# Optimization experiments

Measured on AMD Instinct MI355X. Metric: run time of the kernel, lower is better.

Reference implementation:

```python
import jax, jax.numpy as jnp
import numpy as np

N, E, HID, H, L = 50000, 100000, 128, 4, 3
C = HID          # out_channels per head (concat=True -> H*C = 512)
ED = 1           # edge_dim
HC = H * C


def setup_inputs() -> dict:
    key = jax.random.key(0)
    ks = jax.random.split(key, 20)
    s = 0.05
    w = lambda k, shape: (jax.random.normal(k, shape, jnp.float32) * s)
    inp = {
        'x': jax.random.normal(ks[0], (N, HID), jnp.float32),
        'edge_index': jax.random.randint(ks[1], (2, E), 0, N),
        'edge_attr': jax.random.normal(ks[2], (E, ED), jnp.float32),
        # per-layer stacked parameters (TransformerConv + proj + LayerNorm)
        'Wq': w(ks[3], (L, HID, HC)), 'bq': jnp.zeros((L, HC), jnp.float32),
        'Wk': w(ks[4], (L, HID, HC)), 'bk': jnp.zeros((L, HC), jnp.float32),
        'Wv': w(ks[5], (L, HID, HC)), 'bv': jnp.zeros((L, HC), jnp.float32),
        'We': w(ks[6], (L, ED, HC)),                       # lin_edge, bias=False
        'Wskip': w(ks[7], (L, HID, HC)), 'bskip': jnp.zeros((L, HC), jnp.float32),
        'Wproj': w(ks[8], (L, HC, HID)), 'bproj': jnp.zeros((L, HID), jnp.float32),
        'gamma': jnp.ones((L, HID), jnp.float32), 'beta': jnp.zeros((L, HID), jnp.float32),
    }
    return inp


def reference(x, edge_index, edge_attr, Wq, bq, Wk, bk, Wv, bv, We, Wskip, bskip,
              Wproj, bproj, gamma, beta):
    src, dst = edge_index[0], edge_index[1]
    scale = 1.0 / jnp.sqrt(jnp.asarray(C, x.dtype))
    for l in range(L):
        q = (x @ Wq[l] + bq[l]).reshape(N, H, C)
        k = (x @ Wk[l] + bk[l]).reshape(N, H, C)
        v = (x @ Wv[l] + bv[l]).reshape(N, H, C)
        e = (edge_attr @ We[l]).reshape(E, H, C)
        kj = k[src] + e                                   # [E,H,C]
        alpha = jnp.einsum('ehc,ehc->eh', q[dst], kj) * scale
        # segment softmax over destination nodes
        amax = jax.ops.segment_max(alpha, dst, num_segments=N)
        p = jnp.exp(alpha - amax[dst])
        denom = jax.ops.segment_sum(p, dst, num_segments=N)
        a = p / (denom[dst] + 1e-16)                      # [E,H]
        msg = (v[src] + e) * a[:, :, None]                # [E,H,C]
        agg = jax.ops.segment_sum(msg, dst, num_segments=N).reshape(N, HC)
        conv = agg + x @ Wskip[l] + bskip[l]              # root/skip connection
        h = jax.nn.elu(conv @ Wproj[l] + bproj[l])        # proj + ELU (dropout=eval noop)
        y = x + h                                         # residual
        mu = jnp.mean(y, axis=-1, keepdims=True)
        var = jnp.var(y, axis=-1, keepdims=True)
        x = (y - mu) / jnp.sqrt(var + 1e-5) * gamma[l] + beta[l]
    return x
```

## Files before the change

### kernel.cpp

```cpp
#include <hip/hip_runtime.h>

#define NN 50000
#define NPAD 50176
#define EE 100000
#define HIDD 128
#define HH 4
#define CCC 128
#define HCC 512
#define QS 2048
#define LLL 3
#define SCALE 0.08838834764831845f

typedef unsigned short u16;
typedef unsigned int u32;
typedef __attribute__((ext_vector_type(8))) short bfrag;
typedef __attribute__((ext_vector_type(4))) float fx4;

__device__ __forceinline__ float bfl(u32 u){ return __uint_as_float(u << 16); }
__device__ __forceinline__ float bfh(u32 u){ return __uint_as_float(u & 0xffff0000u); }
__device__ __forceinline__ float bf1(u16 u){ return __uint_as_float((u32)u << 16); }
__device__ __forceinline__ u16 f2bf(float f){
  u32 u = __float_as_uint(f);
  return (u16)((u + 0x7fffu + ((u >> 16) & 1u)) >> 16);
}
__device__ __forceinline__ u32 pack2(float a, float b){
  return (u32)f2bf(a) | ((u32)f2bf(b) << 16);
}

union bfcvt { bfrag f; uint4 u; };

#if defined(__has_builtin)
#if __has_builtin(__builtin_amdgcn_global_load_lds)
#define USE_GLL 1
#endif
#endif
#ifndef USE_GLL
#define USE_GLL 0
#endif

__device__ __forceinline__ void gll16(const u16* g, u16* l){
#if USE_GLL
  __builtin_amdgcn_global_load_lds(
      (const __attribute__((address_space(1))) unsigned int*)(const void*)g,
      (__attribute__((address_space(3))) unsigned int*)(void*)l, 16, 0, 0);
#else
  uint4 v = *(const uint4*)g;
  *(uint4*)l = v;
#endif
}

__global__ __launch_bounds__(256) void kzero(int* p, int n){
  int i = blockIdx.x * 256 + threadIdx.x;
  if (i < n) p[i] = 0;
}

__global__ __launch_bounds__(256) void kcvt(const float* __restrict__ x,
                                            u16* __restrict__ xb){
  int i = blockIdx.x * 256 + threadIdx.x;
  if (i >= NPAD*HIDD/4) return;
  int base = i * 4;
  uint2 o = make_uint2(0u, 0u);
  if (base < NN*HIDD) {
    float4 v = *(const float4*)(x + base);
    o = make_uint2(pack2(v.x,v.y), pack2(v.z,v.w));
  }
  *(uint2*)(xb + base) = o;
}

__global__ __launch_bounds__(256) void khist(const int* __restrict__ ei, int* __restrict__ counts){
  int e = blockIdx.x * 256 + threadIdx.x;
  if (e < EE) atomicAdd(&counts[ei[EE + e]], 1);
}

__global__ __launch_bounds__(256) void kscanA(const int* __restrict__ counts, int* __restrict__ bsum){
  __shared__ int sh[256];
  int t = threadIdx.x, i = blockIdx.x * 256 + t;
  sh[t] = (i < NN) ? counts[i] : 0;
  __syncthreads();
  #pragma unroll
  for (int off = 128; off; off >>= 1) {
    if (t < off) sh[t] += sh[t + off];
    __syncthreads();
  }
  if (t == 0) bsum[blockIdx.x] = sh[0];
}

__global__ __launch_bounds__(256) void kscanB(int* __restrict__ bsum, int nb){
  __shared__ int sh[256];
  int t = threadIdx.x;
  int v = (t < nb) ? bsum[t] : 0;
  sh[t] = v;
  __syncthreads();
  #pragma unroll
  for (int off = 1; off < 256; off <<= 1) {
    int a = (t >= off) ? sh[t - off] : 0;
    __syncthreads();
    sh[t] += a;
    __syncthreads();
  }
  if (t < nb) bsum[t] = sh[t] - v;
}

__global__ __launch_bounds__(256) void kscanC(const int* __restrict__ counts,
                                              const int* __restrict__ bsum,
                                              int* __restrict__ rowptr){
  __shared__ int sh[256];
  int t = threadIdx.x, i = blockIdx.x * 256 + t;
  int v = (i < NN) ? counts[i] : 0;
  sh[t] = v;
  __syncthreads();
  #pragma unroll
  for (int off = 1; off < 256; off <<= 1) {
    int a = (t >= off) ? sh[t - off] : 0;
    __syncthreads();
    sh[t] += a;
    __syncthreads();
  }
  if (i <= NN) rowptr[i] = bsum[blockIdx.x] + sh[t] - v;
}

__global__ __launch_bounds__(256) void kscatter(const int* __restrict__ ei,
                                                const float* __restrict__ ea,
                                                const int* __restrict__ rowptr,
                                                int* __restrict__ fill,
                                                int* __restrict__ csr_src,
                                                float* __restrict__ csr_ea){
  int e = blockIdx.x * 256 + threadIdx.x;
  if (e >= EE) return;
  int d = ei[EE + e];
  int pos = rowptr[d] + atomicAdd(&fill[d], 1);
  csr_src[pos] = ei[e];
  csr_ea[pos]  = ea[e];
}

__global__ __launch_bounds__(256) void kprep(
    const float* __restrict__ Wq, const float* __restrict__ Wk,
    const float* __restrict__ Wv,
    const float* __restrict__ bq, const float* __restrict__ bk,
    const float* __restrict__ bv,
    const float* __restrict__ Wp,
    u16* __restrict__ Wt, u16* __restrict__ Wpt, float* __restrict__ bias_cat)
{
  int id = blockIdx.x * 256 + threadIdx.x;
  if (id < 1536*128) {
    int n = id >> 7, k = id & 127;
    int m = n >> 9, nc = n & 511;
    const float* W = (m==0)?Wq:(m==1)?Wk:Wv;
    Wt[id] = f2bf(W[(size_t)k*HCC + nc]);
  } else if (id < 1536*128 + 128*512) {
    int j = id - 1536*128;
    int n = j >> 9, k = j & 511;
    Wpt[j] = f2bf(Wp[(size_t)k*HIDD + n]);
  } else if (id < 1536*128 + 128*512 + 1536) {
    int n = id - (1536*128 + 128*512);
    int m = n >> 9, nc = n & 511;
    const float* b = (m==0)?bq:(m==1)?bk:bv;
    bias_cat[n] = b[nc];
  }
}

__global__ __launch_bounds__(256) void kskp2(
    const float* __restrict__ Wsk, const u16* __restrict__ Wpt,
    u16* __restrict__ Wskt)
{
  const int t = threadIdx.x;
  const int wave = t >> 6, lane = t & 63;
  const int lo = lane & 15, hi = lane >> 4;
  const int wr = wave >> 1, wc = wave & 1;
  const int b0 = blockIdx.x * 64 + wr * 32;
  const int a0 = blockIdx.y * 32 + wc * 16;

  fx4 acc[2] = {};
  #pragma unroll
  for (int kk = 0; kk < 16; ++kk) {
    const float* wp = Wsk + (size_t)(a0 + lo)*HCC + kk*32 + hi*8;
    float4 u = *(const float4*)(wp);
    float4 w = *(const float4*)(wp + 4);
    bfcvt bc;
    bc.u = make_uint4(pack2(u.x,u.y), pack2(u.z,u.w),
                      pack2(w.x,w.y), pack2(w.z,w.w));
    #pragma unroll
    for (int fr = 0; fr < 2; ++fr) {
      bfrag af = *(const bfrag*)(Wpt + (size_t)(b0 + fr*16 + lo)*HCC + kk*32 + hi*8);
      acc[fr] = __builtin_amdgcn_mfma_f32_16x16x32_bf16(af, bc.f, acc[fr], 0, 0, 0);
    }
  }
  #pragma unroll
  for (int fr = 0; fr < 2; ++fr)
    #pragma unroll
    for (int j = 0; j < 4; ++j)
      Wskt[(size_t)(b0 + fr*16 + hi*4 + j)*128 + a0 + lo] = f2bf(acc[fr][j]);
}

__global__ __launch_bounds__(256) void kbpe(
    const float* __restrict__ bsk, const float* __restrict__ Wp,
    const float* __restrict__ bp, float* __restrict__ bpe)
{
  __shared__ float part[8][32];
  const int c = blockIdx.x * 32 + (threadIdx.x & 31);
  const int seg = threadIdx.x >> 5;
  float s = 0.f;
  #pragma unroll
  for (int j = 0; j < 64; ++j)
    s += bsk[seg*64 + j] * Wp[(size_t)(seg*64 + j)*HIDD + c];
  part[seg][threadIdx.x & 31] = s;
  __syncthreads();
  if (seg == 0) {
    float tot = bp[c];
    #pragma unroll
    for (int k = 0; k < 8; ++k) tot += part[k][threadIdx.x & 31];
    bpe[c] = tot;
  }
}

__global__ __launch_bounds__(256) void k1_mfma(
    const u16* __restrict__ xb, const u16* __restrict__ Wt,
    const float* __restrict__ bias, u16* __restrict__ qkvs)
{
  __shared__ u16 lds[16896];
  const int t = threadIdx.x;
  const int wave = t >> 6, lane = t & 63;
  const int lo = lane & 15, hi = lane >> 4;
  const int wr = wave >> 1, wc = wave & 1;

  int b = blockIdx.x;
  const int qq = 4692/8, rr = 4692%8;
  int xcd = b & 7, slot = b >> 3;
  int wgid = (xcd < rr ? xcd*(qq+1) : rr*(qq+1) + (xcd-rr)*qq) + slot;
  const int rb = (wgid / 12) * 128;
  const int cb = (wgid % 12) * 128;

  auto STAGE = [&](int buf, int kk){
    #pragma unroll
    for (int half = 0; half < 2; ++half) {
      int c = wave*64 + lane + half*256;
      int row = c >> 2, seg = c & 3;
      gll16(xb + (size_t)(rb + row)*HIDD + kk*32 + seg*8,
            &lds[buf*4096 + (wave*64 + half*256)*8]);
    }
    #pragma unroll
    for (int half = 0; half < 2; ++half) {
      int c = wave*64 + lane + half*256;
      int row = c >> 2, seg = c & 3;
      gll16(Wt + (size_t)(cb + row)*HIDD + kk*32 + seg*8,
            &lds[8192 + buf*4096 + (wave*64 + half*256)*8]);
    }
  };

#if !USE_GLL
  auto STAGE_REG = [&](int buf, int kk){
    #pragma unroll
    for (int half = 0; half < 2; ++half) {
      int c = wave*64 + lane + half*256;
      int row = c >> 2, seg = c & 3;
      uint4 v = *(const uint4*)(xb + (size_t)(rb + row)*HIDD + kk*32 + seg*8);
      *(uint4*)&lds[buf*4096 + c*8] = v;
      uint4 w = *(const uint4*)(Wt + (size_t)(cb + row)*HIDD + kk*32 + seg*8);
      *(uint4*)&lds[8192 + buf*4096 + c*8] = w;
    }
  };
#define DO_STAGE STAGE_REG
#else
#define DO_STAGE STAGE
#endif

  fx4 acc[4][4] = {};

  DO_STAGE(0, 0);
  __syncthreads();
  #pragma unroll
  for (int kk = 0; kk < 4; ++kk) {
    const int buf = kk & 1;
    if (kk < 3) DO_STAGE(buf ^ 1, kk + 1);
    bfrag a[4], b2[4];
    #pragma unroll
    for (int fr = 0; fr < 4; ++fr)
      a[fr] = *(const bfrag*)&lds[buf*4096 + (wr*64 + fr*16 + lo)*32 + hi*8];
    #pragma unroll
    for (int fc = 0; fc < 4; ++fc)
      b2[fc] = *(const bfrag*)&lds[8192 + buf*4096 + (wc*64 + fc*16 + lo)*32 + hi*8];
    #pragma unroll
    for (int fr = 0; fr < 4; ++fr)
      #pragma unroll
      for (int fc = 0; fc < 4; ++fc)
        acc[fr][fc] = __builtin_amdgcn_mfma_f32_16x16x32_bf16(a[fr], b2[fc], acc[fr][fc], 0, 0, 0);
    __syncthreads();
  }

  float bb[4];
  #pragma unroll
  for (int fc = 0; fc < 4; ++fc) bb[fc] = bias[cb + wc*64 + fc*16 + lo];
  #pragma unroll
  for (int fr = 0; fr < 4; ++fr)
    #pragma unroll
    for (int fc = 0; fc < 4; ++fc)
      #pragma unroll
      for (int j = 0; j < 4; ++j)
        lds[(size_t)(wr*64 + fr*16 + hi*4 + j)*132 + wc*64 + fc*16 + lo]
            = f2bf(acc[fr][fc][j] + bb[fc]);
  __syncthreads();

  #pragma unroll
  for (int i = 0; i < 8; ++i) {
    int f = t + 256*i;
    int row = f >> 4, seg = f & 15;
    if (rb + row < NN)
      *(uint4*)(qkvs + (size_t)(rb+row)*QS + cb + seg*8) = *(uint4*)&lds[(size_t)row*132 + seg*8];
  }
}

__global__ __launch_bounds__(256) void k23_fused(
    u16* __restrict__ qkvs, const int* __restrict__ rowptr,
    const int* __restrict__ csr_src, const float* __restrict__ csr_ea,
    const float* __restrict__ We)
{
  int wave = threadIdx.x >> 6, lane = threadIdx.x & 63;
  int n = blockIdx.x * 4 + wave;
  if (n >= NN) return;
  int h = lane >> 4, c0 = (lane & 15) * 8;

  uint4 qa = *(const uint4*)(qkvs + (size_t)n*QS + h*CCC + c0);
  float qf[8] = {bfl(qa.x),bfh(qa.x),bfl(qa.y),bfh(qa.y),
                 bfl(qa.z),bfh(qa.z),bfl(qa.w),bfh(qa.w)};
  float4 w0 = *(const float4*)(We + h*CCC + c0);
  float4 w1 = *(const float4*)(We + h*CCC + c0 + 4);
  float wf[8] = {w0.x,w0.y,w0.z,w0.w,w1.x,w1.y,w1.z,w1.w};

  float qw = qf[0]*wf[0]+qf[1]*wf[1]+qf[2]*wf[2]+qf[3]*wf[3]
           + qf[4]*wf[4]+qf[5]*wf[5]+qf[6]*wf[6]+qf[7]*wf[7];
  #pragma unroll
  for (int off = 8; off; off >>= 1) qw += __shfl_xor(qw, off);

  int beg = rowptr[n], end = rowptr[n+1];
  float accv[8] = {};
  float accp = 0.f, accw = 0.f;

  for (int i = beg; i < end; ++i) {
    int src = csr_src[i];
    float eav = csr_ea[i];
    uint4 ka = *(const uint4*)(qkvs + (size_t)src*QS + 512 + h*CCC + c0);
    float s = qf[0]*bfl(ka.x) + qf[1]*bfh(ka.x)
            + qf[2]*bfl(ka.y) + qf[3]*bfh(ka.y)
            + qf[4]*bfl(ka.z) + qf[5]*bfh(ka.z)
            + qf[6]*bfl(ka.w) + qf[7]*bfh(ka.w);
    #pragma unroll
    for (int off = 8; off; off >>= 1) s += __shfl_xor(s, off);
    float p = expf((s + eav * qw) * SCALE);
    uint4 va = *(const uint4*)(qkvs + (size_t)src*QS + 1024 + h*CCC + c0);
    accv[0] += p*bfl(va.x); accv[1] += p*bfh(va.x);
    accv[2] += p*bfl(va.y); accv[3] += p*bfh(va.y);
    accv[4] += p*bfl(va.z); accv[5] += p*bfh(va.z);
    accv[6] += p*bfl(va.w); accv[7] += p*bfh(va.w);
    accp += p; accw += p*eav;
  }

  float inv = 1.f / (accp + 1e-16f);
  float se  = accw * inv;
  u16* ap = qkvs + (size_t)n*QS + 1536 + h*CCC + c0;
  *(uint4*)ap = make_uint4(
    pack2(accv[0]*inv+se*wf[0], accv[1]*inv+se*wf[1]),
    pack2(accv[2]*inv+se*wf[2], accv[3]*inv+se*wf[3]),
    pack2(accv[4]*inv+se*wf[4], accv[5]*inv+se*wf[5]),
    pack2(accv[6]*inv+se*wf[6], accv[7]*inv+se*wf[7]));
}

__global__ __launch_bounds__(256) void k4_mfma(
    const u16* __restrict__ qkvs, const u16* __restrict__ xb_in,
    const u16* __restrict__ Wpt, const u16* __restrict__ Wskt,
    const float* __restrict__ bpe,
    const float* __restrict__ gamma, const float* __restrict__ beta,
    float* __restrict__ x_out, u16* __restrict__ xb_out, int last)
{
  __shared__ __align__(16) u16 lds[10240];
  float* yt   = (float*)lds;
  float* mu_s = (float*)&lds[8448];
  float* rs_s = (float*)&lds[8512];
  const int t = threadIdx.x;
  const int wave = t >> 6, lane = t & 63;
  const int lo = lane & 15, hi = lane >> 4;
  const int wr = wave >> 1, wc = wave & 1;
  const int rb = blockIdx.x * 32;

  auto STAGE = [&](int buf, int kk){
    if (wave < 2) {
      int c = wave*64 + lane;
      int row = c >> 2, seg = c & 3;
      const u16* src = (kk < 16)
        ? qkvs + (size_t)(rb + row)*QS + 1536 + kk*32 + seg*8
        : xb_in + (size_t)(rb + row)*HIDD + (kk-16)*32 + seg*8;
#if USE_GLL
      gll16(src, &lds[buf*1024 + (wave*64)*8]);
#else
      *(uint4*)&lds[buf*1024 + c*8] = *(const uint4*)src;
#endif
    }
    #pragma unroll
    for (int half = 0; half < 2; ++half) {
      int c = wave*64 + lane + half*256;
      int col = c >> 2, seg = c & 3;
      const u16* src = (kk < 16)
        ? Wpt  + (size_t)col*512 + kk*32 + seg*8
        : Wskt + (size_t)col*128 + (kk-16)*32 + seg*8;
#if USE_GLL
      gll16(src, &lds[2048 + buf*4096 + (wave*64 + half*256)*8]);
#else
      *(uint4*)&lds[2048 + buf*4096 + c*8] = *(const uint4*)src;
#endif
    }
  };

  fx4 acc[4] = {};

  STAGE(0, 0);
  __syncthreads();
  #pragma unroll
  for (int kk = 0; kk < 20; ++kk) {
    const int buf = kk & 1;
    if (kk < 19) STAGE(buf ^ 1, kk + 1);
    bfrag a = *(const bfrag*)&lds[buf*1024 + (wr*16 + lo)*32 + hi*8];
    bfrag b[4];
    #pragma unroll
    for (int fc = 0; fc < 4; ++fc)
      b[fc] = *(const bfrag*)&lds[2048 + buf*4096 + (wc*64 + fc*16 + lo)*32 + hi*8];
    #pragma unroll
    for (int fc = 0; fc < 4; ++fc)
      acc[fc] = __builtin_amdgcn_mfma_f32_16x16x32_bf16(a, b[fc], acc[fc], 0, 0, 0);
    __syncthreads();
  }

  float y[4][4];
  #pragma unroll
  for (int fc = 0; fc < 4; ++fc) {
    int col = wc*64 + fc*16 + lo;
    float bb = bpe[col];
    #pragma unroll
    for (int j = 0; j < 4; ++j) {
      int row = rb + wr*16 + hi*4 + j;
      float v = acc[fc][j] + bb;
      v = v > 0.f ? v : expm1f(v);
      float xv = (row < NN) ? bf1(xb_in[(size_t)row*HIDD + col]) : 0.f;
      y[fc][j] = xv + v;
    }
  }
  #pragma unroll
  for (int fc = 0; fc < 4; ++fc)
    #pragma unroll
    for (int j = 0; j < 4; ++j)
      yt[(size_t)(wr*16 + hi*4 + j)*132 + wc*64 + fc*16 + lo] = y[fc][j];
  __syncthreads();

  {
    int r = t >> 3, seg = t & 7;
    float s = 0.f, s2 = 0.f;
    #pragma unroll
    for (int j = 0; j < 16; ++j) {
      float v = yt[(size_t)r*132 + seg*16 + j];
      s += v; s2 += v*v;
    }
    #pragma unroll
    for (int off = 4; off; off >>= 1) { s += __shfl_xor(s, off); s2 += __shfl_xor(s2, off); }
    if (seg == 0) {
      float mu = s * (1.f/128.f);
      float var = s2 * (1.f/128.f) - mu*mu;
      mu_s[r] = mu;
      rs_s[r] = rsqrtf(var + 1e-5f);
    }
  }
  __syncthreads();

  #pragma unroll
  for (int i = 0; i < 4; ++i) {
    int f = t + 256*i;
    int r = f >> 5, c4 = (f & 31) * 4;
    int row = rb + r;
    if (row >= NN) continue;
    float mu = mu_s[r], rs = rs_s[r];
    float4 g  = *(const float4*)(gamma + c4);
    float4 bt = *(const float4*)(beta + c4);
    float4 yv = *(float4*)&yt[(size_t)r*132 + c4];
    float4 o = make_float4((yv.x-mu)*rs*g.x + bt.x, (yv.y-mu)*rs*g.y + bt.y,
                           (yv.z-mu)*rs*g.z + bt.z, (yv.w-mu)*rs*g.w + bt.w);
    *(uint2*)(xb_out + (size_t)row*HIDD + c4) = make_uint2(pack2(o.x,o.y), pack2(o.z,o.w));
    if (last) *(float4*)(x_out + (size_t)row*HIDD + c4) = o;
  }
}

extern "C" void kernel_launch(void* const* d_in, const int* in_sizes, int n_in,
                              void* d_out, int out_size, void* d_ws, size_t ws_size,
                              hipStream_t stream)
{
  const float* x    = (const float*)d_in[0];
  const int*   ei   = (const int*)d_in[1];
  const float* ea   = (const float*)d_in[2];
  const float* Wq   = (const float*)d_in[3];
  const float* bq   = (const float*)d_in[4];
  const float* Wk   = (const float*)d_in[5];
  const float* bk   = (const float*)d_in[6];
  const float* Wv   = (const float*)d_in[7];
  const float* bv   = (const float*)d_in[8];
  const float* We   = (const float*)d_in[9];
  const float* Wsk  = (const float*)d_in[10];
  const float* bsk  = (const float*)d_in[11];
  const float* Wp   = (const float*)d_in[12];
  const float* bp   = (const float*)d_in[13];
  const float* gamma= (const float*)d_in[14];
  const float* beta = (const float*)d_in[15];

  char* wsb = (char*)d_ws;
  size_t off = 0;
  auto alloc = [&](size_t bytes) -> void* {
    void* p = wsb + off;
    off += (bytes + 255) & ~(size_t)255;
    return p;
  };
  u16*   qkvs    = (u16*)  alloc((size_t)NPAD*QS*2);
  u16*   xb      = (u16*)  alloc((size_t)NPAD*HIDD*2);
  int*   rowptr  = (int*)  alloc((size_t)(NN+1)*4);
  int*   counts  = (int*)  alloc((size_t)NN*4);
  int*   fill    = (int*)  alloc((size_t)NN*4);
  int*   bsum    = (int*)  alloc((size_t)256*4);
  int*   csr_src = (int*)  alloc((size_t)EE*4);
  float* csr_ea  = (float*)alloc((size_t)EE*4);
  u16*   Wt      = (u16*)  alloc((size_t)1536*128*2);
  u16*   Wpt     = (u16*)  alloc((size_t)128*512*2);
  u16*   Wskt    = (u16*)  alloc((size_t)128*128*2);
  float* biasc   = (float*)alloc((size_t)1536*4);
  float* bpe     = (float*)alloc((size_t)128*4);
  float* xio     = (float*)d_out;

  const int gn  = (NN + 255)/256;
  const int ge  = (EE + 255)/256;
  const int gp  = (1536*128 + 128*512 + 1536 + 255)/256;
  const int gc  = (NPAD*HIDD/4 + 255)/256;
  const int g1  = 12 * ((NN + 127)/128);
  const dim3 gsk(2, 4);
  const int g23 = (NN + 3)/4;
  const int g4  = NPAD/32;

  kzero<<<gn, 256, 0, stream>>>(counts, NN);
  kzero<<<gn, 256, 0, stream>>>(fill, NN);
  khist<<<ge, 256, 0, stream>>>(ei, counts);
  kscanA<<<gn, 256, 0, stream>>>(counts, bsum);
  kscanB<<<1, 256, 0, stream>>>(bsum, gn);
  kscanC<<<gn, 256, 0, stream>>>(counts, bsum, rowptr);
  kscatter<<<ge, 256, 0, stream>>>(ei, ea, rowptr, fill, csr_src, csr_ea);
  kcvt<<<gc, 256, 0, stream>>>(x, xb);

  for (int l = 0; l < LLL; ++l) {
    const float* Wq_l  = Wq  + (size_t)l*HIDD*HCC;
    const float* Wk_l  = Wk  + (size_t)l*HIDD*HCC;
    const float* Wv_l  = Wv  + (size_t)l*HIDD*HCC;
    const float* Wsk_l = Wsk + (size_t)l*HIDD*HCC;
    const float* bq_l  = bq  + (size_t)l*HCC;
    const float* bk_l  = bk  + (size_t)l*HCC;
    const float* bv_l  = bv  + (size_t)l*HCC;
    const float* bsk_l = bsk + (size_t)l*HCC;
    const float* We_l  = We  + (size_t)l*HCC;
    const float* Wp_l  = Wp  + (size_t)l*HCC*HIDD;
    const float* bp_l  = bp  + (size_t)l*HIDD;
    const float* g_l   = gamma + (size_t)l*HIDD;
    const float* b_l   = beta  + (size_t)l*HIDD;

    kprep<<<gp, 256, 0, stream>>>(Wq_l, Wk_l, Wv_l, bq_l, bk_l, bv_l,
                                  Wp_l, Wt, Wpt, biasc);
    kskp2<<<gsk, 256, 0, stream>>>(Wsk_l, Wpt, Wskt);
    kbpe<<<4, 256, 0, stream>>>(bsk_l, Wp_l, bp_l, bpe);
    k1_mfma<<<g1, 256, 0, stream>>>(xb, Wt, biasc, qkvs);
    k23_fused<<<g23, 256, 0, stream>>>(qkvs, rowptr, csr_src, csr_ea, We_l);
    k4_mfma<<<g4, 256, 0, stream>>>(qkvs, xb, Wpt, Wskt, bpe, g_l, b_l,
                                    xio, xb, (l == LLL-1) ? 1 : 0);
  }
}
```

Measured before the change: 446.1 us.

## Batch weight prep across layers and load A operands directly into registers

Weight preparation kernels (bf16 transpose, Wskip·Wproj fold, bias fold) now run once for all three layers through a grid dimension, replacing three launches per layer. The two zeroing kernels merge into one. In the k1 and k4 GEMMs the A operand (activations) is loaded straight from global memory into MFMA fragments with register double-buffering instead of being staged through LDS, which halves LDS traffic and LDS footprint. This adds register pressure and makes the A loads less coalesced.

Result: slower. 478.0 us (+7.2%).

```diff
diff --git a/kernel.cpp b/kernel.cpp
--- a/kernel.cpp
+++ b/kernel.cpp
@@ -139,30 +139,39 @@
     const float* __restrict__ bq, const float* __restrict__ bk,
     const float* __restrict__ bv,
     const float* __restrict__ Wp,
-    u16* __restrict__ Wt, u16* __restrict__ Wpt, float* __restrict__ bias_cat)
-{
+    u16* __restrict__ Wt3, u16* __restrict__ Wpt3, float* __restrict__ biasc3)
+{
+  const int l = blockIdx.y;
+  const size_t wo = (size_t)l*HIDD*HCC;
+  u16* Wt  = Wt3  + (size_t)l*1536*128;
+  u16* Wpt = Wpt3 + (size_t)l*128*512;
+  float* bias_cat = biasc3 + (size_t)l*1536;
   int id = blockIdx.x * 256 + threadIdx.x;
   if (id < 1536*128) {
     int n = id >> 7, k = id & 127;
     int m = n >> 9, nc = n & 511;
-    const float* W = (m==0)?Wq:(m==1)?Wk:Wv;
+    const float* W = ((m==0)?Wq:(m==1)?Wk:Wv) + wo;
     Wt[id] = f2bf(W[(size_t)k*HCC + nc]);
   } else if (id < 1536*128 + 128*512) {
     int j = id - 1536*128;
     int n = j >> 9, k = j & 511;
-    Wpt[j] = f2bf(Wp[(size_t)k*HIDD + n]);
+    Wpt[j] = f2bf(Wp[wo + (size_t)k*HIDD + n]);
   } else if (id < 1536*128 + 128*512 + 1536) {
     int n = id - (1536*128 + 128*512);
     int m = n >> 9, nc = n & 511;
-    const float* b = (m==0)?bq:(m==1)?bk:bv;
+    const float* b = ((m==0)?bq:(m==1)?bk:bv) + (size_t)l*HCC;
     bias_cat[n] = b[nc];
   }
 }
 
 __global__ __launch_bounds__(256) void kskp2(
-    const float* __restrict__ Wsk, const u16* __restrict__ Wpt,
-    u16* __restrict__ Wskt)
-{
+    const float* __restrict__ Wsk, const u16* __restrict__ Wpt3,
+    u16* __restrict__ Wskt3)
+{
+  const int l = blockIdx.z;
+  const float* WskL = Wsk + (size_t)l*HIDD*HCC;
+  const u16* Wpt = Wpt3 + (size_t)l*128*512;
+  u16* Wskt = Wskt3 + (size_t)l*128*128;
   const int t = threadIdx.x;
   const int wave = t >> 6, lane = t & 63;
   const int lo = lane & 15, hi = lane >> 4;
@@ -173,7 +182,7 @@
   fx4 acc[2] = {};
   #pragma unroll
   for (int kk = 0; kk < 16; ++kk) {
-    const float* wp = Wsk + (size_t)(a0 + lo)*HCC + kk*32 + hi*8;
+    const float* wp = WskL + (size_t)(a0 + lo)*HCC + kk*32 + hi*8;
     float4 u = *(const float4*)(wp);
     float4 w = *(const float4*)(wp + 4);
     bfcvt bc;
@@ -194,22 +203,25 @@
 
 __global__ __launch_bounds__(256) void kbpe(
     const float* __restrict__ bsk, const float* __restrict__ Wp,
-    const float* __restrict__ bp, float* __restrict__ bpe)
+    const float* __restrict__ bp, float* __restrict__ bpe3)
 {
   __shared__ float part[8][32];
+  const int l = blockIdx.y;
+  const float* bskL = bsk + (size_t)l*HCC;
+  const float* WpL  = Wp  + (size_t)l*HCC*HIDD;
   const int c = blockIdx.x * 32 + (threadIdx.x & 31);
   const int seg = threadIdx.x >> 5;
   float s = 0.f;
   #pragma unroll
   for (int j = 0; j < 64; ++j)
-    s += bsk[seg*64 + j] * Wp[(size_t)(seg*64 + j)*HIDD + c];
+    s += bskL[seg*64 + j] * WpL[(size_t)(seg*64 + j)*HIDD + c];
   part[seg][threadIdx.x & 31] = s;
   __syncthreads();
   if (seg == 0) {
-    float tot = bp[c];
+    float tot = bp[(size_t)l*HIDD + c];
     #pragma unroll
     for (int k = 0; k < 8; ++k) tot += part[k][threadIdx.x & 31];
-    bpe[c] = tot;
+    bpe3[(size_t)l*HIDD + c] = tot;
   }
 }
 
@@ -230,61 +242,50 @@
   const int rb = (wgid / 12) * 128;
   const int cb = (wgid % 12) * 128;
 
-  auto STAGE = [&](int buf, int kk){
+  auto STAGE_B = [&](int buf, int kk){
     #pragma unroll
     for (int half = 0; half < 2; ++half) {
       int c = wave*64 + lane + half*256;
       int row = c >> 2, seg = c & 3;
-      gll16(xb + (size_t)(rb + row)*HIDD + kk*32 + seg*8,
+#if USE_GLL
+      gll16(Wt + (size_t)(cb + row)*HIDD + kk*32 + seg*8,
             &lds[buf*4096 + (wave*64 + half*256)*8]);
-    }
-    #pragma unroll
-    for (int half = 0; half < 2; ++half) {
-      int c = wave*64 + lane + half*256;
-      int row = c >> 2, seg = c & 3;
-      gll16(Wt + (size_t)(cb + row)*HIDD + kk*32 + seg*8,
-            &lds[8192 + buf*4096 + (wave*64 + half*256)*8]);
+#else
+      *(uint4*)&lds[buf*4096 + c*8] = *(const uint4*)(Wt + (size_t)(cb + row)*HIDD + kk*32 + seg*8);
+#endif
     }
   };
-
-#if !USE_GLL
-  auto STAGE_REG = [&](int buf, int kk){
-    #pragma unroll
-    for (int half = 0; half < 2; ++half) {
-      int c = wave*64 + lane + half*256;
-      int row = c >> 2, seg = c & 3;
-      uint4 v = *(const uint4*)(xb + (size_t)(rb + row)*HIDD + kk*32 + seg*8);
-      *(uint4*)&lds[buf*4096 + c*8] = v;
-      uint4 w = *(const uint4*)(Wt + (size_t)(cb + row)*HIDD + kk*32 + seg*8);
-      *(uint4*)&lds[8192 + buf*4096 + c*8] = w;
+  auto LDA = [&](int kk, bfrag* dst){
+    #pragma unroll
+    for (int fr = 0; fr < 4; ++fr) {
+      bfcvt cv;
+      cv.u = *(const uint4*)(xb + (size_t)(rb + wr*64 + fr*16 + lo)*HIDD + kk*32 + hi*8);
+      dst[fr] = cv.f;
     }
   };
-#define DO_STAGE STAGE_REG
-#else
-#define DO_STAGE STAGE
-#endif
 
   fx4 acc[4][4] = {};
-
-  DO_STAGE(0, 0);
+  bfrag aCur[4], aNxt[4];
+
+  LDA(0, aCur);
+  STAGE_B(0, 0);
   __syncthreads();
   #pragma unroll
   for (int kk = 0; kk < 4; ++kk) {
     const int buf = kk & 1;
-    if (kk < 3) DO_STAGE(buf ^ 1, kk + 1);
-    bfrag a[4], b2[4];
-    #pragma unroll
-    for (int fr = 0; fr < 4; ++fr)
-      a[fr] = *(const bfrag*)&lds[buf*4096 + (wr*64 + fr*16 + lo)*32 + hi*8];
+    if (kk < 3) { LDA(kk + 1, aNxt); STAGE_B(buf ^ 1, kk + 1); }
+    bfrag b2[4];
     #pragma unroll
     for (int fc = 0; fc < 4; ++fc)
-      b2[fc] = *(const bfrag*)&lds[8192 + buf*4096 + (wc*64 + fc*16 + lo)*32 + hi*8];
+      b2[fc] = *(const bfrag*)&lds[buf*4096 + (wc*64 + fc*16 + lo)*32 + hi*8];
     #pragma unroll
     for (int fr = 0; fr < 4; ++fr)
       #pragma unroll
       for (int fc = 0; fc < 4; ++fc)
-        acc[fr][fc] = __builtin_amdgcn_mfma_f32_16x16x32_bf16(a[fr], b2[fc], acc[fr][fc], 0, 0, 0);
-    __syncthreads();
+        acc[fr][fc] = __builtin_amdgcn_mfma_f32_16x16x32_bf16(aCur[fr], b2[fc], acc[fr][fc], 0, 0, 0);
+    __syncthreads();
+    #pragma unroll
+    for (int fr = 0; fr < 4; ++fr) aCur[fr] = aNxt[fr];
   }
 
   float bb[4];
@@ -371,29 +372,17 @@
     const float* __restrict__ gamma, const float* __restrict__ beta,
     float* __restrict__ x_out, u16* __restrict__ xb_out, int last)
 {
-  __shared__ __align__(16) u16 lds[10240];
-  float* yt   = (float*)lds;
-  float* mu_s = (float*)&lds[8448];
-  float* rs_s = (float*)&lds[8512];
+  __shared__ __align__(16) u16 lds[8448];
+  __shared__ float mu_s[32], rs_s[32];
+  float* yt = (float*)lds;
   const int t = threadIdx.x;
   const int wave = t >> 6, lane = t & 63;
   const int lo = lane & 15, hi = lane >> 4;
   const int wr = wave >> 1, wc = wave & 1;
   const int rb = blockIdx.x * 32;
-
-  auto STAGE = [&](int buf, int kk){
-    if (wave < 2) {
-      int c = wave*64 + lane;
-      int row = c >> 2, seg = c & 3;
-      const u16* src = (kk < 16)
-        ? qkvs + (size_t)(rb + row)*QS + 1536 + kk*32 + seg*8
-        : xb_in + (size_t)(rb + row)*HIDD + (kk-16)*32 + seg*8;
-#if USE_GLL
-      gll16(src, &lds[buf*1024 + (wave*64)*8]);
-#else
-      *(uint4*)&lds[buf*1024 + c*8] = *(const uint4*)src;
-#endif
-    }
+  const int arow = rb + wr*16 + lo;
+
+  auto STAGE_B = [&](int buf, int kk){
     #pragma unroll
     for (int half = 0; half < 2; ++half) {
       int c = wave*64 + lane + half*256;
@@ -402,30 +391,38 @@
         ? Wpt  + (size_t)col*512 + kk*32 + seg*8
         : Wskt + (size_t)col*128 + (kk-16)*32 + seg*8;
 #if USE_GLL
-      gll16(src, &lds[2048 + buf*4096 + (wave*64 + half*256)*8]);
+      gll16(src, &lds[buf*4096 + (wave*64 + half*256)*8]);
 #else
-      *(uint4*)&lds[2048 + buf*4096 + c*8] = *(const uint4*)src;
+      *(uint4*)&lds[buf*4096 + c*8] = *(const uint4*)src;
 #endif
     }
   };
+  auto LDA = [&](int kk)->bfrag{
+    const u16* src = (kk < 16)
+      ? qkvs + (size_t)arow*QS + 1536 + kk*32 + hi*8
+      : xb_in + (size_t)arow*HIDD + (kk-16)*32 + hi*8;
+    bfcvt cv; cv.u = *(const uint4*)src; return cv.f;
+  };
 
   fx4 acc[4] = {};
-
-  STAGE(0, 0);
+  bfrag aCur, aNxt;
+
+  aCur = LDA(0);
+  STAGE_B(0, 0);
   __syncthreads();
   #pragma unroll
   for (int kk = 0; kk < 20; ++kk) {
     const int buf = kk & 1;
-    if (kk < 19) STAGE(buf ^ 1, kk + 1);
-    bfrag a = *(const bfrag*)&lds[buf*1024 + (wr*16 + lo)*32 + hi*8];
+    if (kk < 19) { aNxt = LDA(kk + 1); STAGE_B(buf ^ 1, kk + 1); }
     bfrag b[4];
     #pragma unroll
     for (int fc = 0; fc < 4; ++fc)
-      b[fc] = *(const bfrag*)&lds[2048 + buf*4096 + (wc*64 + fc*16 + lo)*32 + hi*8];
+      b[fc] = *(const bfrag*)&lds[buf*4096 + (wc*64 + fc*16 + lo)*32 + hi*8];
     #pragma unroll
     for (int fc = 0; fc < 4; ++fc)
-      acc[fc] = __builtin_amdgcn_mfma_f32_16x16x32_bf16(a, b[fc], acc[fc], 0, 0, 0);
-    __syncthreads();
+      acc[fc] = __builtin_amdgcn_mfma_f32_16x16x32_bf16(aCur, b[fc], acc[fc], 0, 0, 0);
+    __syncthreads();
+    aCur = aNxt;
   }
 
   float y[4][4];
@@ -516,58 +513,51 @@
   u16*   qkvs    = (u16*)  alloc((size_t)NPAD*QS*2);
   u16*   xb      = (u16*)  alloc((size_t)NPAD*HIDD*2);
   int*   rowptr  = (int*)  alloc((size_t)(NN+1)*4);
-  int*   counts  = (int*)  alloc((size_t)NN*4);
-  int*   fill    = (int*)  alloc((size_t)NN*4);
+  int*   cntfill = (int*)  alloc((size_t)2*NN*4);
+  int*   counts  = cntfill;
+  int*   fill    = cntfill + NN;
   int*   bsum    = (int*)  alloc((size_t)256*4);
   int*   csr_src = (int*)  alloc((size_t)EE*4);
   float* csr_ea  = (float*)alloc((size_t)EE*4);
-  u16*   Wt      = (u16*)  alloc((size_t)1536*128*2);
-  u16*   Wpt     = (u16*)  alloc((size_t)128*512*2);
-  u16*   Wskt    = (u16*)  alloc((size_t)128*128*2);
-  float* biasc   = (float*)alloc((size_t)1536*4);
-  float* bpe     = (float*)alloc((size_t)128*4);
+  u16*   Wt3     = (u16*)  alloc((size_t)3*1536*128*2);
+  u16*   Wpt3    = (u16*)  alloc((size_t)3*128*512*2);
+  u16*   Wskt3   = (u16*)  alloc((size_t)3*128*128*2);
+  float* biasc3  = (float*)alloc((size_t)3*1536*4);
+  float* bpe3    = (float*)alloc((size_t)3*128*4);
   float* xio     = (float*)d_out;
 
   const int gn  = (NN + 255)/256;
+  const int gz  = (2*NN + 255)/256;
   const int ge  = (EE + 255)/256;
-  const int gp  = (1536*128 + 128*512 + 1536 + 255)/256;
   const int gc  = (NPAD*HIDD/4 + 255)/256;
+  const dim3 gp((1536*128 + 128*512 + 1536 + 255)/256, 3);
+  const dim3 gsk(2, 4, 3);
+  const dim3 gbp(4, 3);
   const int g1  = 12 * ((NN + 127)/128);
-  const dim3 gsk(2, 4);
   const int g23 = (NN + 3)/4;
   const int g4  = NPAD/32;
 
-  kzero<<<gn, 256, 0, stream>>>(counts, NN);
-  kzero<<<gn, 256, 0, stream>>>(fill, NN);
+  kzero<<<gz, 256, 0, stream>>>(cntfill, 2*NN);
   khist<<<ge, 256, 0, stream>>>(ei, counts);
   kscanA<<<gn, 256, 0, stream>>>(counts, bsum);
   kscanB<<<1, 256, 0, stream>>>(bsum, gn);
   kscanC<<<gn, 256, 0, stream>>>(counts, bsum, rowptr);
   kscatter<<<ge, 256, 0, stream>>>(ei, ea, rowptr, fill, csr_src, csr_ea);
   kcvt<<<gc, 256, 0, stream>>>(x, xb);
+  kprep<<<gp, 256, 0, stream>>>(Wq, Wk, Wv, bq, bk, bv, Wp, Wt3, Wpt3, biasc3);
+  kskp2<<<gsk, 256, 0, stream>>>(Wsk, Wpt3, Wskt3);
+  kbpe<<<gbp, 256, 0, stream>>>(bsk, Wp, bp, bpe3);
 
   for (int l = 0; l < LLL; ++l) {
-    const float* Wq_l  = Wq  + (size_t)l*HIDD*HCC;
-    const float* Wk_l  = Wk  + (size_t)l*HIDD*HCC;
-    const float* Wv_l  = Wv  + (size_t)l*HIDD*HCC;
-    const float* Wsk_l = Wsk + (size_t)l*HIDD*HCC;
-    const float* bq_l  = bq  + (size_t)l*HCC;
-    const float* bk_l  = bk  + (size_t)l*HCC;
-    const float* bv_l  = bv  + (size_t)l*HCC;
-    const float* bsk_l = bsk + (size_t)l*HCC;
-    const float* We_l  = We  + (size_t)l*HCC;
-    const float* Wp_l  = Wp  + (size_t)l*HCC*HIDD;
-    const float* bp_l  = bp  + (size_t)l*HIDD;
-    const float* g_l   = gamma + (size_t)l*HIDD;
-    const float* b_l   = beta  + (size_t)l*HIDD;
-
-    kprep<<<gp, 256, 0, stream>>>(Wq_l, Wk_l, Wv_l, bq_l, bk_l, bv_l,
-                                  Wp_l, Wt, Wpt, biasc);
-    kskp2<<<gsk, 256, 0, stream>>>(Wsk_l, Wpt, Wskt);
-    kbpe<<<4, 256, 0, stream>>>(bsk_l, Wp_l, bp_l, bpe);
-    k1_mfma<<<g1, 256, 0, stream>>>(xb, Wt, biasc, qkvs);
+    const float* We_l = We + (size_t)l*HCC;
+    const float* g_l  = gamma + (size_t)l*HIDD;
+    const float* b_l  = beta  + (size_t)l*HIDD;
+
+    k1_mfma<<<g1, 256, 0, stream>>>(xb, Wt3 + (size_t)l*1536*128,
+                                    biasc3 + (size_t)l*1536, qkvs);
     k23_fused<<<g23, 256, 0, stream>>>(qkvs, rowptr, csr_src, csr_ea, We_l);
-    k4_mfma<<<g4, 256, 0, stream>>>(qkvs, xb, Wpt, Wskt, bpe, g_l, b_l,
-                                    xio, xb, (l == LLL-1) ? 1 : 0);
-  }
-}
+    k4_mfma<<<g4, 256, 0, stream>>>(qkvs, xb, Wpt3 + (size_t)l*128*512,
+                                    Wskt3 + (size_t)l*128*128, bpe3 + (size_t)l*128,
+                                    g_l, b_l, xio, xb, (l == LLL-1) ? 1 : 0);
+  }
+}
```
